# Kernel tuning notes

Hardware: AMD Instinct MI355X
Metric: run time of the kernel (lower is better)

Reference implementation:

```python
import jax, jax.numpy as jnp
import numpy as np

# Config constants matching init_kwargs (layer_no=2 -> stride 8, anch_mask=[0,1,2])
ANCHORS = np.array([[10,13],[16,30],[33,23],[30,61],[62,45],[59,119],
                    [116,90],[156,198],[373,326]], np.float32)
STRIDE = 8.0
N_CLASSES = 80
A = 3          # n_anchors in this head
IGNORE = 0.7   # ignore_thre
LAMBDA = 0.5


def _forward(xin, labels, W, b):
    B = xin.shape[0]
    F = xin.shape[2]
    n_ch = 5 + N_CLASSES
    anchors = jnp.asarray(ANCHORS) / STRIDE      # all_anchors_grid, [9,2]
    m_anch = anchors[:A]                         # masked_anchors (anch_mask=[0,1,2])

    # 1x1 conv -> [B, A, F, F, n_ch]
    out = jnp.einsum('bchw,oc->bohw', xin, W) + b[None, :, None, None]
    out = out.reshape(B, A, n_ch, F, F).transpose(0, 1, 3, 4, 2)
    ch = jnp.arange(n_ch)
    output = jnp.where((ch < 2) | (ch >= 4), jax.nn.sigmoid(out), out)

    # box decode (pred); only [..., :4] is used (detached) for IoU ignore mask
    xs = jnp.arange(F, dtype=xin.dtype)
    pred_x = output[..., 0] + xs                 # x varies along last spatial axis
    pred_y = output[..., 1] + xs[:, None]        # y varies along rows
    pred_w = jnp.exp(output[..., 2]) * m_anch[:, 0][None, :, None, None]
    pred_h = jnp.exp(output[..., 3]) * m_anch[:, 1][None, :, None, None]
    pred4 = jax.lax.stop_gradient(jnp.stack([pred_x, pred_y, pred_w, pred_h], -1))

    lab = jax.lax.stop_gradient(labels)          # original uses labels.cpu().data
    valid = lab.sum(-1) > 0                      # [B,K]
    tx = lab[..., 1] * F
    ty = lab[..., 2] * F
    tw = lab[..., 3] * F
    th = lab[..., 4] * F
    ti = tx.astype(jnp.int32)
    tj = ty.astype(jnp.int32)
    tbox = jnp.stack([tx, ty, tw, th], -1)       # [B,K,4]

    # anchor matching: bboxes_iou(truth_box, ref_anchors) with xyxy=True, faithful to source
    ref = jnp.concatenate([jnp.zeros_like(anchors), anchors], -1)   # [9,4] = [0,0,w,h]
    tl = jnp.maximum(tbox[..., None, :2], ref[:, :2])
    br = jnp.minimum(tbox[..., None, 2:], ref[:, 2:])
    area_a = jnp.prod(tbox[..., 2:] - tbox[..., :2], -1)            # [B,K]
    area_b = anchors[:, 0] * anchors[:, 1]                          # [9]
    ai = jnp.prod(br - tl, -1) * jnp.all(tl < br, -1)
    a_iou = ai / (area_a[..., None] + area_b - ai)                  # [B,K,9]
    a_iou = jnp.where(valid[..., None], a_iou, -1.0)
    best_all = jnp.argmax(a_iou, -1)                                # [B,K]
    best_mask = best_all < A                                        # in anch_mask {0,1,2}
    best_n = best_all % A

    # pred-vs-truth IoU (xywh) -> objectness ignore mask
    p = pred4.reshape(B, -1, 4)                                     # [B, A*F*F, 4]
    ptl = p[..., :2] - p[..., 2:] * 0.5
    pbr = p[..., :2] + p[..., 2:] * 0.5
    ttl = tbox[..., :2] - tbox[..., 2:] * 0.5
    tbr = tbox[..., :2] + tbox[..., 2:] * 0.5
    tl2 = jnp.maximum(ptl[:, :, None], ttl[:, None])                # [B,N,K,2]
    br2 = jnp.minimum(pbr[:, :, None], tbr[:, None])
    ai2 = jnp.prod(br2 - tl2, -1) * jnp.all(tl2 < br2, -1)
    denom = (p[..., 2] * p[..., 3])[:, :, None] + (tbox[..., 2] * tbox[..., 3])[:, None, :] - ai2
    piou = jnp.where(valid[:, None, :], ai2 / denom, 0.0)
    obj_mask = 1.0 - (piou.max(-1) > IGNORE).astype(xin.dtype).reshape(B, A, F, F)

    # vectorized scatter of per-truth-box assignments
    assign = valid & best_mask
    bidx = jnp.broadcast_to(jnp.arange(B)[:, None], valid.shape)
    lin = ((bidx * A + best_n) * F + tj) * F + ti
    ncells = B * A * F * F
    lin = jnp.where(assign, lin, ncells).reshape(-1)    # OOB rows dropped in scatter

    aw = m_anch[best_n, 0]
    ah = m_anch[best_n, 1]
    onehot = jax.nn.one_hot(lab[..., 0].astype(jnp.int32), N_CLASSES, dtype=xin.dtype)
    tvec = jnp.concatenate([
        (tx - ti)[..., None], (ty - tj)[..., None],
        jnp.log(tw / aw + 1e-16)[..., None], jnp.log(th / ah + 1e-16)[..., None],
        jnp.ones_like(tx)[..., None], onehot], -1).reshape(-1, n_ch)
    scale = jnp.sqrt(2.0 - tw * th / (F * F))           # [B,K]

    obj_mask = obj_mask.reshape(-1).at[lin].set(1.0, mode='drop').reshape(B, A, F, F)
    tgt_mask = jnp.zeros((ncells, 4 + N_CLASSES), xin.dtype).at[lin].set(1.0, mode='drop')
    tgt_mask = tgt_mask.reshape(B, A, F, F, 4 + N_CLASSES)
    tgt_scale = jnp.zeros((ncells, 2), xin.dtype).at[lin].set(
        jnp.stack([scale, scale], -1).reshape(-1, 2), mode='drop').reshape(B, A, F, F, 2)
    target = jnp.zeros((ncells, n_ch), xin.dtype).at[lin].set(tvec, mode='drop')
    target = target.reshape(B, A, F, F, n_ch)

    def process(x):
        xy = x[..., :2] * tgt_mask[..., :2]
        wh = x[..., 2:4] * tgt_mask[..., 2:4] * tgt_scale
        obj = (x[..., 4] * obj_mask)[..., None]
        cl = x[..., 5:] * tgt_mask[..., 4:]
        return jnp.concatenate([xy, wh, obj, cl], -1)

    o = process(output)
    t = process(target)

    def bce(p_, t_, w=None):
        # torch BCELoss clamps log terms at -100
        l = -(t_ * jnp.maximum(jnp.log(p_), -100.0)
              + (1.0 - t_) * jnp.maximum(jnp.log(1.0 - p_), -100.0))
        return (l * w if w is not None else l).sum()

    loss_xy = bce(o[..., :2], t[..., :2], tgt_scale * tgt_scale)
    loss_wh = LAMBDA * ((o[..., 2:4] - t[..., 2:4]) ** 2).sum()
    loss_obj = bce(o[..., 4], t[..., 4])
    loss_cls = bce(o[..., 5:], t[..., 5:])
    loss_l2 = ((o - t) ** 2).sum()
    loss = loss_xy + loss_wh + loss_obj + loss_cls
    return jnp.stack([loss, loss_xy, loss_wh, loss_obj, loss_cls, loss_l2])


def setup_inputs() -> dict:
    key = jax.random.key(0)
    k1, k2, k3, k4, k5 = jax.random.split(key, 5)
    B, C, F, K = 16, 256, 76, 40
    n_ch = 5 + N_CLASSES
    xin = jax.random.normal(k1, (B, C, F, F), jnp.float32)
    W = jax.random.normal(k2, (A * n_ch, C), jnp.float32) * 0.02  # 1x1 conv weight
    b = jnp.zeros((A * n_ch,), jnp.float32)
    cls = jax.random.randint(k3, (B, K, 1), 0, N_CLASSES).astype(jnp.float32)
    xy = jax.random.uniform(k4, (B, K, 2), jnp.float32, 0.05, 0.95)
    wh = jax.random.uniform(k5, (B, K, 2), jnp.float32, 0.02, 0.4)
    labels = jnp.concatenate([cls, xy, wh], -1)   # [B,K,5] = [class,xc,yc,w,h]
    return {"xin": xin, "labels": labels, "W": W, "b": b}


def reference(xin, labels, W, b):
    return _forward(xin, labels, W, b)
```

## Files before the change

### kernel.cpp

```cpp
#include <hip/hip_runtime.h>
#include <math.h>

typedef unsigned int u32;
typedef unsigned short u16;
typedef __attribute__((ext_vector_type(4))) u32 u32x4;
typedef __attribute__((ext_vector_type(8))) short bf16x8;
typedef __attribute__((ext_vector_type(4))) float f32x4;

#define FDIM 76
#define NCELL 5776
#define NA 3
#define NCH 85
#define NCLS 80
#define KLAB 40
#define NB 16
#define CIN 256
#define TILES_PER_B 91
#define NBLK (NB * TILES_PER_B)
#define CS_LD 68

typedef __attribute__((address_space(1))) const void gvoid_t;
typedef __attribute__((address_space(3))) void svoid_t;

__device__ __forceinline__ float sigmf_(float x) { return __frcp_rn(1.0f + __expf(-x)); }
__device__ __forceinline__ float bce_fullf(float p, float t) {
    return -(t * fmaxf(__logf(p), -100.0f) + (1.0f - t) * fmaxf(__logf(1.0f - p), -100.0f));
}
__device__ __forceinline__ float bce1f(float p) { return -fmaxf(__logf(p), -100.0f); }
__device__ __forceinline__ float bce0f(float p) { return -fmaxf(__logf(1.0f - p), -100.0f); }

__device__ __forceinline__ u16 bf16rne(float f) {
    u32 u = __float_as_uint(f);
    u32 r = u + 0x7fffu + ((u >> 16) & 1u);
    return (u16)(r >> 16);
}
__device__ __forceinline__ float bf16f(u16 v) { return __uint_as_float(((u32)v) << 16); }

__global__ __launch_bounds__(256) void yolo_wconv(const float* __restrict__ W,
                                                  u16* __restrict__ Wbf) {
    int idx = blockIdx.x * 256 + threadIdx.x;
    int row = idx >> 8, col = idx & 255;
    float v = (row < NA * NCH) ? W[row * CIN + col] : 0.0f;
    Wbf[idx] = bf16rne(v);
}

__global__ __launch_bounds__(64) void yolo_lab(const float* __restrict__ labels,
                                               float* __restrict__ lrec) {
    int idx = blockIdx.x * 64 + threadIdx.x;
    if (idx >= NB * KLAB) return;
    const float* l = labels + idx * 5;
    float cls = l[0], x = l[1], y = l[2], ww = l[3], hh = l[4];
    bool valid = (cls + x + y + ww + hh) > 0.0f;
    float tx = x * FDIM, ty = y * FDIM, tw = ww * FDIM, th = hh * FDIM;
    int ti = (int)tx, tj = (int)ty;
    float area_a = (tw - tx) * (th - ty);
    const float aw[9] = {1.25f, 2.0f, 4.125f, 3.75f, 7.75f, 7.375f, 14.5f, 19.5f, 46.625f};
    const float ah[9] = {1.625f, 3.75f, 2.875f, 7.625f, 5.625f, 14.875f, 11.25f, 24.75f, 40.75f};
    float best = -1e30f;
    int bi = 0;
    for (int n = 0; n < 9; n++) {
        float bw = fminf(tw, aw[n]), bh = fminf(th, ah[n]);
        float ai = ((tx < bw) && (ty < bh)) ? (bw - tx) * (bh - ty) : 0.0f;
        float iou = valid ? ai / (area_a + aw[n] * ah[n] - ai) : -1.0f;
        if (iou > best) { best = iou; bi = n; }
    }
    int bn = bi % 3;
    bool assign = valid && (bi < 3);
    float* r = lrec + idx * 16;
    r[0] = tx - 0.5f * tw; r[1] = ty - 0.5f * th;
    r[2] = tx + 0.5f * tw; r[3] = ty + 0.5f * th;
    r[4] = tw * th;
    r[5] = valid ? 1.0f : 0.0f;
    r[6] = assign ? (float)((bn * FDIM + tj) * FDIM + ti) : -1.0f;
    r[7] = sqrtf(2.0f - tw * th / (float)(FDIM * FDIM));
    r[8] = tx - (float)ti; r[9] = ty - (float)tj;
    r[10] = logf(tw / aw[bn] + 1e-16f); r[11] = logf(th / ah[bn] + 1e-16f);
    r[12] = cls; r[13] = 0.0f; r[14] = 0.0f; r[15] = 0.0f;
}

__global__ __launch_bounds__(512, 6) void yolo_mfma(const float* __restrict__ xin,
                                                    const u16* __restrict__ Wbf,
                                                    const float* __restrict__ bias,
                                                    const float* __restrict__ lrec,
                                                    float* __restrict__ partials) {
    __shared__ char smem[43776];
    float* S0  = (float*)smem;
    float* S1  = (float*)(smem + 16384);
    u16*   A   = (u16*)(smem + 32768);
    u16*   Csb = (u16*)smem;
    float* Lb  = (float*)(smem + 40960);
    float* red = (float*)(smem + 43520);

    const int blk = blockIdx.x;
    const int b = blk / TILES_PER_B;
    const int tile = blk - b * TILES_PER_B;
    const int cell0 = tile * 64;
    const int t = threadIdx.x;
    const int lane = t & 63;
    const int wid = t >> 6;
    const int g = lane >> 4;
    const int l15 = lane & 15;

    const float* xbase = xin + (size_t)b * CIN * NCELL;
    const int cg0 = cell0 + lane;
    const int cg = cg0 < NCELL ? cg0 : NCELL - 1;

    for (int i = t; i < KLAB * 16; i += 512) Lb[i] = lrec[b * KLAB * 16 + i];

#pragma unroll
    for (int i = 0; i < 8; i++) {
        const int kl = wid * 8 + i;
        __builtin_amdgcn_global_load_lds(
            (gvoid_t*)(xbase + (size_t)kl * NCELL + cg),
            (svoid_t*)(S0 + kl * 64), 4, 0, 0);
    }

    f32x4 acc[2][4];
#pragma unroll
    for (int mi = 0; mi < 2; mi++)
#pragma unroll
        for (int ni = 0; ni < 4; ni++) acc[mi][ni] = (f32x4){0.f, 0.f, 0.f, 0.f};

    const u16* wrow = Wbf + (wid * 32 + l15) * CIN;

#pragma unroll
    for (int c = 0; c < 4; c++) {
        float* Sc = (c & 1) ? S1 : S0;
        bf16x8 af[4];
#pragma unroll
        for (int s2 = 0; s2 < 2; s2++)
#pragma unroll
            for (int mi = 0; mi < 2; mi++)
                af[s2 * 2 + mi] = *(const bf16x8*)(wrow + mi * 16 * CIN + c * 64 + s2 * 32 + g * 8);
        if (c < 3) {
            float* Sn = (c & 1) ? S0 : S1;
#pragma unroll
            for (int i = 0; i < 8; i++) {
                const int kl = wid * 8 + i;
                __builtin_amdgcn_global_load_lds(
                    (gvoid_t*)(xbase + (size_t)((c + 1) * 64 + kl) * NCELL + cg),
                    (svoid_t*)(Sn + kl * 64), 4, 0, 0);
            }
            asm volatile("s_waitcnt vmcnt(8) lgkmcnt(0)" ::: "memory");
        } else {
            asm volatile("s_waitcnt vmcnt(0) lgkmcnt(0)" ::: "memory");
        }
        __builtin_amdgcn_sched_barrier(0);
        __builtin_amdgcn_s_barrier();
        __builtin_amdgcn_sched_barrier(0);
        {
            const float* sp = Sc + wid * 8 * 64 + lane;
            u32x4 v;
#pragma unroll
            for (int e = 0; e < 4; e++) {
                float f0 = sp[(2 * e) * 64];
                float f1 = sp[(2 * e + 1) * 64];
                v[e] = (u32)bf16rne(f0) | ((u32)bf16rne(f1) << 16);
            }
            const int byte = (lane * 128 + wid * 16) ^ ((lane & 7) << 4);
            *(u32x4*)((char*)A + byte) = v;
        }
        asm volatile("s_waitcnt lgkmcnt(0)" ::: "memory");
        __builtin_amdgcn_sched_barrier(0);
        __builtin_amdgcn_s_barrier();
        __builtin_amdgcn_sched_barrier(0);
#pragma unroll
        for (int s2 = 0; s2 < 2; s2++) {
#pragma unroll
            for (int ni = 0; ni < 4; ni++) {
                const int cell = ni * 16 + l15;
                const int byte = (cell * 128 + s2 * 64 + g * 16) ^ ((cell & 7) << 4);
                bf16x8 bfr = *(const bf16x8*)((char*)A + byte);
                acc[0][ni] = __builtin_amdgcn_mfma_f32_16x16x32_bf16(af[s2 * 2 + 0], bfr, acc[0][ni], 0, 0, 0);
                acc[1][ni] = __builtin_amdgcn_mfma_f32_16x16x32_bf16(af[s2 * 2 + 1], bfr, acc[1][ni], 0, 0, 0);
            }
        }
    }

    __syncthreads();

    float bv[8];
#pragma unroll
    for (int mi = 0; mi < 2; mi++)
#pragma unroll
        for (int reg = 0; reg < 4; reg++) {
            const int ch = wid * 32 + mi * 16 + g * 4 + reg;
            bv[mi * 4 + reg] = (ch < NA * NCH) ? bias[ch] : 0.0f;
        }
#pragma unroll
    for (int mi = 0; mi < 2; mi++)
#pragma unroll
        for (int ni = 0; ni < 4; ni++)
#pragma unroll
            for (int reg = 0; reg < 4; reg++) {
                const int ch = wid * 32 + mi * 16 + g * 4 + reg;
                const int cell = ni * 16 + l15;
                Csb[ch * CS_LD + cell] = bf16rne(acc[mi][ni][reg] + bv[mi * 4 + reg]);
            }
    __syncthreads();

    float part[5] = {0.f, 0.f, 0.f, 0.f, 0.f};
    if (t < 384) {
        const int half = (t >= 192) ? 1 : 0;
        const int unit = t - half * 192;
        const int a = unit >> 6;
        const int c = unit & 63;
        const int cgl = cell0 + c;
        if (cgl < NCELL) {
            const int chb = a * NCH;
            const int hh = cgl / FDIM;
            const int ww = cgl - hh * FDIM;
            const float mykey = (float)((a * FDIM + hh) * FDIM + ww);
            if (half == 0) {
                float v0 = bf16f(Csb[(chb + 0) * CS_LD + c]);
                float v1 = bf16f(Csb[(chb + 1) * CS_LD + c]);
                float v2 = bf16f(Csb[(chb + 2) * CS_LD + c]);
                float v3 = bf16f(Csb[(chb + 3) * CS_LD + c]);
                float v4 = bf16f(Csb[(chb + 4) * CS_LD + c]);
                const float manw[3] = {1.25f, 2.0f, 4.125f};
                const float manh[3] = {1.625f, 3.75f, 2.875f};
                float s0 = sigmf_(v0), s1 = sigmf_(v1), s4 = sigmf_(v4);
                float pw = __expf(v2) * manw[a];
                float ph = __expf(v3) * manh[a];
                float px = s0 + (float)ww, py = s1 + (float)hh;
                float parea = pw * ph;
                float ptlx = px - 0.5f * pw, ptly = py - 0.5f * ph;
                float pbrx = px + 0.5f * pw, pbry = py + 0.5f * ph;
                float maxiou = -1e30f;
                int aidx = -1;
                for (int k = 0; k < KLAB; k++) {
                    const f32x4 Aq = *(const f32x4*)&Lb[k * 16];
                    const f32x4 Bq = *(const f32x4*)&Lb[k * 16 + 4];
                    float tlx = fmaxf(ptlx, Aq.x), tly = fmaxf(ptly, Aq.y);
                    float brx = fminf(pbrx, Aq.z), bry = fminf(pbry, Aq.w);
                    float inter = ((tlx < brx) && (tly < bry)) ? (brx - tlx) * (bry - tly) : 0.0f;
                    float iou = (Bq.y != 0.0f) ? inter * __frcp_rn(parea + Bq.x - inter) : 0.0f;
                    maxiou = fmaxf(maxiou, iou);
                    if (Bq.z == mykey) aidx = k;
                }
                if (aidx >= 0) {
                    const f32x4 Bq = *(const f32x4*)&Lb[aidx * 16 + 4];
                    const f32x4 Tv = *(const f32x4*)&Lb[aidx * 16 + 8];
                    float sc = Bq.w, sc2 = sc * sc;
                    part[0] += sc2 * (bce_fullf(s0, Tv.x) + bce_fullf(s1, Tv.y));
                    float dw = v2 - Tv.z, dh = v3 - Tv.w;
                    float whq = dw * dw + dh * dh;
                    part[1] += 0.5f * sc2 * whq;
                    part[2] += bce1f(s4);
                    int ci = (int)Lb[aidx * 16 + 12];
                    float l2 = (s0 - Tv.x) * (s0 - Tv.x) + (s1 - Tv.y) * (s1 - Tv.y) +
                               sc2 * whq + (s4 - 1.0f) * (s4 - 1.0f);
                    float lcls = 0.0f;
                    for (int cc = 0; cc < 40; cc++) {
                        float s = sigmf_(bf16f(Csb[(chb + 5 + cc) * CS_LD + c]));
                        if (cc == ci) { lcls += bce1f(s); l2 += (s - 1.0f) * (s - 1.0f); }
                        else          { lcls += bce0f(s); l2 += s * s; }
                    }
                    part[3] += lcls; part[4] += l2;
                } else {
                    bool objm = !(maxiou > 0.7f);
                    if (objm) { part[2] += bce0f(s4); part[4] += s4 * s4; }
                }
            } else {
                int aidx = -1;
                for (int k = 0; k < KLAB; k++) {
                    const f32x4 Bq = *(const f32x4*)&Lb[k * 16 + 4];
                    if (Bq.z == mykey) aidx = k;
                }
                if (aidx >= 0) {
                    int ci = (int)Lb[aidx * 16 + 12];
                    float lcls = 0.0f, l2 = 0.0f;
                    for (int cc = 40; cc < 80; cc++) {
                        float s = sigmf_(bf16f(Csb[(chb + 5 + cc) * CS_LD + c]));
                        if (cc == ci) { lcls += bce1f(s); l2 += (s - 1.0f) * (s - 1.0f); }
                        else          { lcls += bce0f(s); l2 += s * s; }
                    }
                    part[3] += lcls; part[4] += l2;
                }
            }
        }
    }

#pragma unroll
    for (int i = 0; i < 5; i++) {
        float v = part[i];
        for (int off = 32; off > 0; off >>= 1) v += __shfl_down(v, off);
        if ((t & 63) == 0) red[(t >> 6) * 8 + i] = v;
    }
    __syncthreads();
    if (t == 0) {
#pragma unroll
        for (int i = 0; i < 5; i++) {
            float s = red[i];
#pragma unroll
            for (int wv = 1; wv < 8; wv++) s += red[wv * 8 + i];
            partials[blk * 8 + i] = s;
        }
    }
}

__global__ __launch_bounds__(256) void yolo_fin(const float* __restrict__ partials,
                                                float* __restrict__ out, int n) {
    __shared__ float red[4][8];
    const int t = threadIdx.x;
    float s[5] = {0.f, 0.f, 0.f, 0.f, 0.f};
    for (int r = t; r < n; r += 256)
#pragma unroll
        for (int i = 0; i < 5; i++) s[i] += partials[r * 8 + i];
#pragma unroll
    for (int i = 0; i < 5; i++) {
        float v = s[i];
        for (int off = 32; off > 0; off >>= 1) v += __shfl_down(v, off);
        if ((t & 63) == 0) red[t >> 6][i] = v;
    }
    __syncthreads();
    if (t == 0) {
        float xy  = red[0][0] + red[1][0] + red[2][0] + red[3][0];
        float wh  = red[0][1] + red[1][1] + red[2][1] + red[3][1];
        float obj = red[0][2] + red[1][2] + red[2][2] + red[3][2];
        float cls = red[0][3] + red[1][3] + red[2][3] + red[3][3];
        float l2  = red[0][4] + red[1][4] + red[2][4] + red[3][4];
        out[0] = xy + wh + obj + cls;
        out[1] = xy; out[2] = wh; out[3] = obj; out[4] = cls; out[5] = l2;
    }
}

extern "C" void kernel_launch(void* const* d_in, const int* in_sizes, int n_in,
                              void* d_out, int out_size, void* d_ws, size_t ws_size,
                              hipStream_t stream) {
    const float* xin    = (const float*)d_in[0];
    const float* labels = (const float*)d_in[1];
    const float* Wm     = (const float*)d_in[2];
    const float* bias   = (const float*)d_in[3];
    float* out = (float*)d_out;

    float* partials = (float*)d_ws;
    float* lrec  = (float*)((char*)d_ws + 46592);
    u16*   Wbf   = (u16*)((char*)d_ws + 46592 + 40960);

    yolo_wconv<<<256, 256, 0, stream>>>(Wm, Wbf);
    yolo_lab<<<(NB * KLAB + 63) / 64, 64, 0, stream>>>(labels, lrec);
    yolo_mfma<<<NBLK, 512, 0, stream>>>(xin, Wbf, bias, lrec, partials);
    yolo_fin<<<1, 256, 0, stream>>>(partials, out, NBLK);
}
```

Baseline: 73.54 us.

## Merge weight-convert and label-prep kernels; read label records from global memory

Combines the bf16 weight conversion and the label preprocessing into one launch, using an extra block for the labels, which removes one kernel launch and its gap. The main kernel no longer copies the per-image label records into LDS. It reads them straight from global memory, relying on cache hits and uniform addresses, which shrinks shared memory per block and may raise occupancy. The cost is that the 40-iteration IoU loop now issues global or scalar loads instead of LDS reads, and these can have higher latency.

```diff
diff --git a/kernel.cpp b/kernel.cpp
--- a/kernel.cpp
+++ b/kernel.cpp
@@ -36,46 +36,47 @@
 }
 __device__ __forceinline__ float bf16f(u16 v) { return __uint_as_float(((u32)v) << 16); }
 
-__global__ __launch_bounds__(256) void yolo_wconv(const float* __restrict__ W,
-                                                  u16* __restrict__ Wbf) {
-    int idx = blockIdx.x * 256 + threadIdx.x;
-    int row = idx >> 8, col = idx & 255;
-    float v = (row < NA * NCH) ? W[row * CIN + col] : 0.0f;
-    Wbf[idx] = bf16rne(v);
-}
-
-__global__ __launch_bounds__(64) void yolo_lab(const float* __restrict__ labels,
-                                               float* __restrict__ lrec) {
-    int idx = blockIdx.x * 64 + threadIdx.x;
-    if (idx >= NB * KLAB) return;
-    const float* l = labels + idx * 5;
-    float cls = l[0], x = l[1], y = l[2], ww = l[3], hh = l[4];
-    bool valid = (cls + x + y + ww + hh) > 0.0f;
-    float tx = x * FDIM, ty = y * FDIM, tw = ww * FDIM, th = hh * FDIM;
-    int ti = (int)tx, tj = (int)ty;
-    float area_a = (tw - tx) * (th - ty);
-    const float aw[9] = {1.25f, 2.0f, 4.125f, 3.75f, 7.75f, 7.375f, 14.5f, 19.5f, 46.625f};
-    const float ah[9] = {1.625f, 3.75f, 2.875f, 7.625f, 5.625f, 14.875f, 11.25f, 24.75f, 40.75f};
-    float best = -1e30f;
-    int bi = 0;
-    for (int n = 0; n < 9; n++) {
-        float bw = fminf(tw, aw[n]), bh = fminf(th, ah[n]);
-        float ai = ((tx < bw) && (ty < bh)) ? (bw - tx) * (bh - ty) : 0.0f;
-        float iou = valid ? ai / (area_a + aw[n] * ah[n] - ai) : -1.0f;
-        if (iou > best) { best = iou; bi = n; }
-    }
-    int bn = bi % 3;
-    bool assign = valid && (bi < 3);
-    float* r = lrec + idx * 16;
-    r[0] = tx - 0.5f * tw; r[1] = ty - 0.5f * th;
-    r[2] = tx + 0.5f * tw; r[3] = ty + 0.5f * th;
-    r[4] = tw * th;
-    r[5] = valid ? 1.0f : 0.0f;
-    r[6] = assign ? (float)((bn * FDIM + tj) * FDIM + ti) : -1.0f;
-    r[7] = sqrtf(2.0f - tw * th / (float)(FDIM * FDIM));
-    r[8] = tx - (float)ti; r[9] = ty - (float)tj;
-    r[10] = logf(tw / aw[bn] + 1e-16f); r[11] = logf(th / ah[bn] + 1e-16f);
-    r[12] = cls; r[13] = 0.0f; r[14] = 0.0f; r[15] = 0.0f;
+__global__ __launch_bounds__(256) void yolo_prep(const float* __restrict__ W,
+                                                 const float* __restrict__ labels,
+                                                 u16* __restrict__ Wbf,
+                                                 float* __restrict__ lrec) {
+    if (blockIdx.x < 256) {
+        int idx = blockIdx.x * 256 + threadIdx.x;
+        int row = idx >> 8, col = idx & 255;
+        float v = (row < NA * NCH) ? W[row * CIN + col] : 0.0f;
+        Wbf[idx] = bf16rne(v);
+        return;
+    }
+    for (int idx = threadIdx.x; idx < NB * KLAB; idx += 256) {
+        const float* l = labels + idx * 5;
+        float cls = l[0], x = l[1], y = l[2], ww = l[3], hh = l[4];
+        bool valid = (cls + x + y + ww + hh) > 0.0f;
+        float tx = x * FDIM, ty = y * FDIM, tw = ww * FDIM, th = hh * FDIM;
+        int ti = (int)tx, tj = (int)ty;
+        float area_a = (tw - tx) * (th - ty);
+        const float aw[9] = {1.25f, 2.0f, 4.125f, 3.75f, 7.75f, 7.375f, 14.5f, 19.5f, 46.625f};
+        const float ah[9] = {1.625f, 3.75f, 2.875f, 7.625f, 5.625f, 14.875f, 11.25f, 24.75f, 40.75f};
+        float best = -1e30f;
+        int bi = 0;
+        for (int n = 0; n < 9; n++) {
+            float bw = fminf(tw, aw[n]), bh = fminf(th, ah[n]);
+            float ai = ((tx < bw) && (ty < bh)) ? (bw - tx) * (bh - ty) : 0.0f;
+            float iou = valid ? ai / (area_a + aw[n] * ah[n] - ai) : -1.0f;
+            if (iou > best) { best = iou; bi = n; }
+        }
+        int bn = bi % 3;
+        bool assign = valid && (bi < 3);
+        float* r = lrec + idx * 16;
+        r[0] = tx - 0.5f * tw; r[1] = ty - 0.5f * th;
+        r[2] = tx + 0.5f * tw; r[3] = ty + 0.5f * th;
+        r[4] = tw * th;
+        r[5] = valid ? 1.0f : 0.0f;
+        r[6] = assign ? (float)((bn * FDIM + tj) * FDIM + ti) : -1.0f;
+        r[7] = sqrtf(2.0f - tw * th / (float)(FDIM * FDIM));
+        r[8] = tx - (float)ti; r[9] = ty - (float)tj;
+        r[10] = logf(tw / aw[bn] + 1e-16f); r[11] = logf(th / ah[bn] + 1e-16f);
+        r[12] = cls; r[13] = 0.0f; r[14] = 0.0f; r[15] = 0.0f;
+    }
 }
 
 __global__ __launch_bounds__(512, 6) void yolo_mfma(const float* __restrict__ xin,
@@ -83,13 +84,12 @@
                                                     const float* __restrict__ bias,
                                                     const float* __restrict__ lrec,
                                                     float* __restrict__ partials) {
-    __shared__ char smem[43776];
+    __shared__ char smem[40960];
     float* S0  = (float*)smem;
     float* S1  = (float*)(smem + 16384);
     u16*   A   = (u16*)(smem + 32768);
     u16*   Csb = (u16*)smem;
-    float* Lb  = (float*)(smem + 40960);
-    float* red = (float*)(smem + 43520);
+    float* red = (float*)(smem + 40704);
 
     const int blk = blockIdx.x;
     const int b = blk / TILES_PER_B;
@@ -102,10 +102,9 @@
     const int l15 = lane & 15;
 
     const float* xbase = xin + (size_t)b * CIN * NCELL;
+    const float* lb = lrec + b * KLAB * 16;
     const int cg0 = cell0 + lane;
     const int cg = cg0 < NCELL ? cg0 : NCELL - 1;
-
-    for (int i = t; i < KLAB * 16; i += 512) Lb[i] = lrec[b * KLAB * 16 + i];
 
 #pragma unroll
     for (int i = 0; i < 8; i++) {
@@ -229,8 +228,8 @@
                 float maxiou = -1e30f;
                 int aidx = -1;
                 for (int k = 0; k < KLAB; k++) {
-                    const f32x4 Aq = *(const f32x4*)&Lb[k * 16];
-                    const f32x4 Bq = *(const f32x4*)&Lb[k * 16 + 4];
+                    const f32x4 Aq = *(const f32x4*)(lb + k * 16);
+                    const f32x4 Bq = *(const f32x4*)(lb + k * 16 + 4);
                     float tlx = fmaxf(ptlx, Aq.x), tly = fmaxf(ptly, Aq.y);
                     float brx = fminf(pbrx, Aq.z), bry = fminf(pbry, Aq.w);
                     float inter = ((tlx < brx) && (tly < bry)) ? (brx - tlx) * (bry - tly) : 0.0f;
@@ -239,15 +238,15 @@
                     if (Bq.z == mykey) aidx = k;
                 }
                 if (aidx >= 0) {
-                    const f32x4 Bq = *(const f32x4*)&Lb[aidx * 16 + 4];
-                    const f32x4 Tv = *(const f32x4*)&Lb[aidx * 16 + 8];
+                    const f32x4 Bq = *(const f32x4*)(lb + aidx * 16 + 4);
+                    const f32x4 Tv = *(const f32x4*)(lb + aidx * 16 + 8);
                     float sc = Bq.w, sc2 = sc * sc;
                     part[0] += sc2 * (bce_fullf(s0, Tv.x) + bce_fullf(s1, Tv.y));
                     float dw = v2 - Tv.z, dh = v3 - Tv.w;
                     float whq = dw * dw + dh * dh;
                     part[1] += 0.5f * sc2 * whq;
                     part[2] += bce1f(s4);
-                    int ci = (int)Lb[aidx * 16 + 12];
+                    int ci = (int)lb[aidx * 16 + 12];
                     float l2 = (s0 - Tv.x) * (s0 - Tv.x) + (s1 - Tv.y) * (s1 - Tv.y) +
                                sc2 * whq + (s4 - 1.0f) * (s4 - 1.0f);
                     float lcls = 0.0f;
@@ -264,11 +263,10 @@
             } else {
                 int aidx = -1;
                 for (int k = 0; k < KLAB; k++) {
-                    const f32x4 Bq = *(const f32x4*)&Lb[k * 16 + 4];
-                    if (Bq.z == mykey) aidx = k;
+                    if (lb[k * 16 + 6] == mykey) aidx = k;
                 }
                 if (aidx >= 0) {
-                    int ci = (int)Lb[aidx * 16 + 12];
+                    int ci = (int)lb[aidx * 16 + 12];
                     float lcls = 0.0f, l2 = 0.0f;
                     for (int cc = 40; cc < 80; cc++) {
                         float s = sigmf_(bf16f(Csb[(chb + 5 + cc) * CS_LD + c]));
@@ -338,8 +336,7 @@
     float* lrec  = (float*)((char*)d_ws + 46592);
     u16*   Wbf   = (u16*)((char*)d_ws + 46592 + 40960);
 
-    yolo_wconv<<<256, 256, 0, stream>>>(Wm, Wbf);
-    yolo_lab<<<(NB * KLAB + 63) / 64, 64, 0, stream>>>(labels, lrec);
+    yolo_prep<<<257, 256, 0, stream>>>(Wm, labels, Wbf, lrec);
     yolo_mfma<<<NBLK, 512, 0, stream>>>(xin, Wbf, bias, lrec, partials);
     yolo_fin<<<1, 256, 0, stream>>>(partials, out, NBLK);
 }
```

Result: faster. 70.97 us (-3.5%).
